# Kernel tuning notes

Measured on AMD Instinct MI355X. Metric: run time of the kernel, lower is better.

The kernel has to match this reference:

```python
import jax, jax.numpy as jnp
import numpy as np

B, S, D = 2, 2048, 1024
H, HD = 16, 64
DFF = 4 * D
EPS = 1e-5


def gelu(x):
    return 0.5 * x * (1.0 + jnp.tanh(jnp.sqrt(2.0 / jnp.pi) * (x + 0.044715 * x * x * x)))


def layer_norm(x, scale, bias):
    mu = jnp.mean(x, axis=-1, keepdims=True)
    var = jnp.mean(jnp.square(x - mu), axis=-1, keepdims=True)
    return (x - mu) * jax.lax.rsqrt(var + EPS) * scale + bias


def setup_inputs() -> dict:
    key = jax.random.key(0)
    ks = jax.random.split(key, 8)
    s = 0.02
    x = jax.random.normal(ks[0], (B, S, D), jnp.float32)
    mask = jnp.tril(jnp.ones((S, S), dtype=bool))[None, None]  # (1,1,S,S) causal
    return {
        "x": x,
        "mask": mask,
        "ln1_scale": jnp.ones((D,), jnp.float32),
        "ln1_bias": jnp.zeros((D,), jnp.float32),
        "ln2_scale": jnp.ones((D,), jnp.float32),
        "ln2_bias": jnp.zeros((D,), jnp.float32),
        "w_qkv": jax.random.normal(ks[1], (D, 3 * D), jnp.float32) * s,
        "b_qkv": jnp.zeros((3 * D,), jnp.float32),
        "w_attn_proj": jax.random.normal(ks[2], (D, D), jnp.float32) * s,
        "b_attn_proj": jnp.zeros((D,), jnp.float32),
        "w_fc": jax.random.normal(ks[3], (D, DFF), jnp.float32) * s,
        "b_fc": jnp.zeros((DFF,), jnp.float32),
        "w_mlp_proj": jax.random.normal(ks[4], (DFF, D), jnp.float32) * s,
        "b_mlp_proj": jnp.zeros((D,), jnp.float32),
    }


def reference(x, mask, ln1_scale, ln1_bias, ln2_scale, ln2_bias,
              w_qkv, b_qkv, w_attn_proj, b_attn_proj,
              w_fc, b_fc, w_mlp_proj, b_mlp_proj):
    bsz, seq, _ = x.shape
    # --- attention branch ---
    h = layer_norm(x, ln1_scale, ln1_bias)
    qkv = h @ w_qkv + b_qkv                       # (b, s, 3D)
    q, k, v = jnp.split(qkv, 3, axis=-1)
    q = q.reshape(bsz, seq, H, HD).transpose(0, 2, 1, 3)  # bhsd
    k = k.reshape(bsz, seq, H, HD).transpose(0, 2, 1, 3)
    v = v.reshape(bsz, seq, H, HD).transpose(0, 2, 1, 3)
    q = q * (1.0 / jnp.sqrt(HD))
    scores = jnp.einsum('bhqd,bhkd->bhqk', q, k)
    scores = jnp.where(mask, scores, -1e10)
    probs = jax.nn.softmax(scores, axis=-1)
    attn = jnp.einsum('bhqk,bhkd->bhqd', probs, v)
    attn = attn.transpose(0, 2, 1, 3).reshape(bsz, seq, D)
    attn = attn @ w_attn_proj + b_attn_proj
    x = x + attn
    # --- MLP branch ---
    h = layer_norm(x, ln2_scale, ln2_bias)
    h = gelu(h @ w_fc + b_fc)
    h = h @ w_mlp_proj + b_mlp_proj
    return x + h
```

## Files before the change

kernel.cpp:

```cpp
#include <hip/hip_runtime.h>
#include <stdint.h>


typedef __attribute__((ext_vector_type(8))) short bf16x8;
typedef __attribute__((ext_vector_type(8))) unsigned short u16x8;
typedef __attribute__((ext_vector_type(4))) float f32x4;

#define NEG_BIG -30000.0f
#define EXP2SC 0.18033688011112042f

__device__ __forceinline__ float b2f(unsigned short u) {
  union { unsigned int i; float f; } c; c.i = ((unsigned int)u) << 16; return c.f;
}
__device__ __forceinline__ unsigned short f2b(float f) {
  union { float f; unsigned int u; } c; c.f = f;
  unsigned int r = c.u + 0x7fffu + ((c.u >> 16) & 1u);
  return (unsigned short)(r >> 16);
}
__device__ __forceinline__ float ldx(const void* p, size_t i, int f32) {
  return f32 ? ((const float*)p)[i] : b2f(((const unsigned short*)p)[i]);
}
__device__ __forceinline__ void gld_lds16(const void* g, void* l) {
  __builtin_amdgcn_global_load_lds(
      (__attribute__((address_space(1))) void*)(void*)g,
      (__attribute__((address_space(3))) void*)l, 16, 0, 0);
}

__global__ void detect_k(const unsigned short* __restrict__ x, int* __restrict__ flag) {
  int lane = threadIdx.x;
  int cnt = 0;
#pragma unroll
  for (int j = 0; j < 4; ++j) {
    unsigned e = (x[lane * 4 + j] >> 7) & 0xFF;
    if (e >= 100 && e <= 145) cnt++;
  }
#pragma unroll
  for (int off = 32; off; off >>= 1) cnt += __shfl_down(cnt, off);
  if (lane == 0) *flag = (cnt < 220) ? 1 : 0;
}

__global__ __launch_bounds__(256) void transpose_k(
    const void* __restrict__ in, unsigned short* __restrict__ out,
    int K, int N, const int* __restrict__ flag) {
  int fm = *flag;
  __shared__ unsigned short tile[64][72];
  int n0 = blockIdx.x * 64, k0 = blockIdx.y * 64;
  int t = threadIdx.x;
  int r = t >> 3, c0 = (t & 7) * 8;
  if (fm) {
    const float* inf = (const float*)in;
#pragma unroll
    for (int p = 0; p < 2; ++p) {
      int k = r + p * 32;
      float4 v0 = *(const float4*)(inf + (size_t)(k0 + k) * N + n0 + c0);
      float4 v1 = *(const float4*)(inf + (size_t)(k0 + k) * N + n0 + c0 + 4);
      tile[k][c0 + 0] = f2b(v0.x); tile[k][c0 + 1] = f2b(v0.y);
      tile[k][c0 + 2] = f2b(v0.z); tile[k][c0 + 3] = f2b(v0.w);
      tile[k][c0 + 4] = f2b(v1.x); tile[k][c0 + 5] = f2b(v1.y);
      tile[k][c0 + 6] = f2b(v1.z); tile[k][c0 + 7] = f2b(v1.w);
    }
  } else {
    const unsigned short* inu = (const unsigned short*)in;
#pragma unroll
    for (int p = 0; p < 2; ++p) {
      int k = r + p * 32;
      u16x8 v = *(const u16x8*)(inu + (size_t)(k0 + k) * N + n0 + c0);
      *(u16x8*)&tile[k][c0] = v;
    }
  }
  __syncthreads();
#pragma unroll
  for (int p = 0; p < 2; ++p) {
    int n = r + p * 32;
    u16x8 v;
#pragma unroll
    for (int j = 0; j < 8; ++j) v[j] = tile[c0 + j][n];
    *(u16x8*)(out + (size_t)(n0 + n) * K + k0 + c0) = v;
  }
}

__global__ __launch_bounds__(256) void ln_k(
    const void* __restrict__ x, const void* __restrict__ sc,
    const void* __restrict__ bs, unsigned short* __restrict__ out,
    const int* __restrict__ flag, int xAdap) {
  int fm = *flag;
  int fx = xAdap ? fm : 0;
  int row = blockIdx.x, t = threadIdx.x;
  float f0, f1, f2, f3;
  if (fx) {
    float4 xv = ((const float4*)x)[(size_t)row * 256 + t];
    f0 = xv.x; f1 = xv.y; f2 = xv.z; f3 = xv.w;
  } else {
    ushort4 xv = ((const ushort4*)x)[(size_t)row * 256 + t];
    f0 = b2f(xv.x); f1 = b2f(xv.y); f2 = b2f(xv.z); f3 = b2f(xv.w);
  }
  float s = f0 + f1 + f2 + f3;
  float q = f0 * f0 + f1 * f1 + f2 * f2 + f3 * f3;
#pragma unroll
  for (int off = 32; off; off >>= 1) {
    s += __shfl_down(s, off);
    q += __shfl_down(q, off);
  }
  __shared__ float red[8];
  int w = t >> 6, lane = t & 63;
  if (lane == 0) { red[w] = s; red[w + 4] = q; }
  __syncthreads();
  float S = red[0] + red[1] + red[2] + red[3];
  float Q = red[4] + red[5] + red[6] + red[7];
  float mean = S * (1.f / 1024.f);
  float var = Q * (1.f / 1024.f) - mean * mean;
  float rstd = rsqrtf(var + 1e-5f);
  int c = t * 4;
  ushort4 o;
  o.x = f2b((f0 - mean) * rstd * ldx(sc, c, fm)     + ldx(bs, c, fm));
  o.y = f2b((f1 - mean) * rstd * ldx(sc, c + 1, fm) + ldx(bs, c + 1, fm));
  o.z = f2b((f2 - mean) * rstd * ldx(sc, c + 2, fm) + ldx(bs, c + 2, fm));
  o.w = f2b((f3 - mean) * rstd * ldx(sc, c + 3, fm) + ldx(bs, c + 3, fm));
  ((ushort4*)(out + (size_t)row * 1024))[t] = o;
}

template <int EPI>
__global__ __launch_bounds__(256) void gemm_bt(
    const unsigned short* __restrict__ A, const unsigned short* __restrict__ Bt,
    const void* __restrict__ bias, const void* __restrict__ res,
    void* __restrict__ C, int M, int N, int K,
    const int* __restrict__ flag, int resAdap, int outAdap) {
  int fm = *flag;
  int fr = resAdap ? fm : 0;
  int fo = outAdap ? fm : 0;
  __shared__ unsigned short As[2][128 * 32];
  __shared__ unsigned short Bs[2][128 * 32];
  int t = threadIdx.x;
  int bn = blockIdx.x * 128, bm = blockIdx.y * 128;
  int w = t >> 6, lane = t & 63, quad = lane >> 4, l16 = lane & 15;
  int wm = (w >> 1) * 64, wn = (w & 1) * 64;
  f32x4 acc[4][4] = {};

  int c1 = t, c2 = t + 256;
  int r1 = c1 >> 2, e1 = (c1 & 3) * 8;
  int r2 = c2 >> 2, e2 = (c2 & 3) * 8;
  const unsigned short* a1 = A + (size_t)(bm + r1) * K + e1;
  const unsigned short* a2 = A + (size_t)(bm + r2) * K + e2;
  const unsigned short* b1 = Bt + (size_t)(bn + r1) * K + e1;
  const unsigned short* b2 = Bt + (size_t)(bn + r2) * K + e2;

  for (int k0 = 0; k0 < K; k0 += 64) {
    gld_lds16(a1 + k0,      As[0] + c1 * 8);
    gld_lds16(a2 + k0,      As[0] + c2 * 8);
    gld_lds16(a1 + k0 + 32, As[1] + c1 * 8);
    gld_lds16(a2 + k0 + 32, As[1] + c2 * 8);
    gld_lds16(b1 + k0,      Bs[0] + c1 * 8);
    gld_lds16(b2 + k0,      Bs[0] + c2 * 8);
    gld_lds16(b1 + k0 + 32, Bs[1] + c1 * 8);
    gld_lds16(b2 + k0 + 32, Bs[1] + c2 * 8);
    __syncthreads();
#pragma unroll
    for (int h = 0; h < 2; ++h) {
      bf16x8 af[4], bfr[4];
#pragma unroll
      for (int i = 0; i < 4; ++i)
        af[i] = *(const bf16x8*)&As[h][(wm + i * 16 + l16) * 32 + quad * 8];
#pragma unroll
      for (int j = 0; j < 4; ++j)
        bfr[j] = *(const bf16x8*)&Bs[h][(wn + j * 16 + l16) * 32 + quad * 8];
#pragma unroll
      for (int i = 0; i < 4; ++i)
#pragma unroll
        for (int j = 0; j < 4; ++j)
          acc[i][j] = __builtin_amdgcn_mfma_f32_16x16x32_bf16(af[i], bfr[j], acc[i][j], 0, 0, 0);
    }
    __syncthreads();
  }

#pragma unroll
  for (int j = 0; j < 4; ++j) {
    int col = bn + wn + j * 16 + l16;
    float bb = ldx(bias, col, fm);
#pragma unroll
    for (int i = 0; i < 4; ++i) {
      int row0 = bm + wm + i * 16 + quad * 4;
#pragma unroll
      for (int r = 0; r < 4; ++r) {
        float v = acc[i][j][r] + bb;
        if (EPI == 1) {
          float u = 0.7978845608f * (v + 0.044715f * v * v * v);
          float e = __expf(2.f * u);
          float th = 1.f - 2.f / (e + 1.f);
          v = 0.5f * v * (1.f + th);
        } else if (EPI == 2) {
          v += ldx(res, (size_t)(row0 + r) * N + col, fr);
        }
        size_t idx = (size_t)(row0 + r) * N + col;
        if (fo) ((float*)C)[idx] = v;
        else    ((unsigned short*)C)[idx] = f2b(v);
      }
    }
  }
}

__global__ __launch_bounds__(256) void gemm_pk(
    const unsigned short* __restrict__ A, const unsigned short* __restrict__ Bt,
    float* __restrict__ P, int M, int N, int Kh, int Kfull) {
  __shared__ unsigned short As[2][128 * 32];
  __shared__ unsigned short Bs[2][128 * 32];
  int t = threadIdx.x;
  int bn = blockIdx.x * 128, bm = blockIdx.y * 128;
  int koff = blockIdx.z * Kh;
  float* Pz = P + (size_t)blockIdx.z * M * N;
  int w = t >> 6, lane = t & 63, quad = lane >> 4, l16 = lane & 15;
  int wm = (w >> 1) * 64, wn = (w & 1) * 64;
  f32x4 acc[4][4] = {};

  int c1 = t, c2 = t + 256;
  int r1 = c1 >> 2, e1 = (c1 & 3) * 8;
  int r2 = c2 >> 2, e2 = (c2 & 3) * 8;
  const unsigned short* a1 = A + (size_t)(bm + r1) * Kfull + koff + e1;
  const unsigned short* a2 = A + (size_t)(bm + r2) * Kfull + koff + e2;
  const unsigned short* b1 = Bt + (size_t)(bn + r1) * Kfull + koff + e1;
  const unsigned short* b2 = Bt + (size_t)(bn + r2) * Kfull + koff + e2;

  for (int k0 = 0; k0 < Kh; k0 += 64) {
    gld_lds16(a1 + k0,      As[0] + c1 * 8);
    gld_lds16(a2 + k0,      As[0] + c2 * 8);
    gld_lds16(a1 + k0 + 32, As[1] + c1 * 8);
    gld_lds16(a2 + k0 + 32, As[1] + c2 * 8);
    gld_lds16(b1 + k0,      Bs[0] + c1 * 8);
    gld_lds16(b2 + k0,      Bs[0] + c2 * 8);
    gld_lds16(b1 + k0 + 32, Bs[1] + c1 * 8);
    gld_lds16(b2 + k0 + 32, Bs[1] + c2 * 8);
    __syncthreads();
#pragma unroll
    for (int h = 0; h < 2; ++h) {
      bf16x8 af[4], bfr[4];
#pragma unroll
      for (int i = 0; i < 4; ++i)
        af[i] = *(const bf16x8*)&As[h][(wm + i * 16 + l16) * 32 + quad * 8];
#pragma unroll
      for (int j = 0; j < 4; ++j)
        bfr[j] = *(const bf16x8*)&Bs[h][(wn + j * 16 + l16) * 32 + quad * 8];
#pragma unroll
      for (int i = 0; i < 4; ++i)
#pragma unroll
        for (int j = 0; j < 4; ++j)
          acc[i][j] = __builtin_amdgcn_mfma_f32_16x16x32_bf16(af[i], bfr[j], acc[i][j], 0, 0, 0);
    }
    __syncthreads();
  }

#pragma unroll
  for (int j = 0; j < 4; ++j) {
    int col = bn + wn + j * 16 + l16;
#pragma unroll
    for (int i = 0; i < 4; ++i) {
      int row0 = bm + wm + i * 16 + quad * 4;
#pragma unroll
      for (int r = 0; r < 4; ++r)
        Pz[(size_t)(row0 + r) * N + col] = acc[i][j][r];
    }
  }
}

__global__ __launch_bounds__(256) void reduce2_k(
    const float* __restrict__ P0, const float* __restrict__ P1,
    const void* __restrict__ bias, const void* __restrict__ res,
    void* __restrict__ out, int N,
    const int* __restrict__ flag, int resAdap, int outAdap) {
  int fm = *flag;
  int fr = resAdap ? fm : 0;
  int fo = outAdap ? fm : 0;
  size_t idx = ((size_t)blockIdx.x * 256 + threadIdx.x) * 4;
  float4 p0 = *(const float4*)(P0 + idx);
  float4 p1 = *(const float4*)(P1 + idx);
  int col = (int)(idx & (size_t)(N - 1));
  float v0 = p0.x + p1.x + ldx(bias, col, fm)     + ldx(res, idx, fr);
  float v1 = p0.y + p1.y + ldx(bias, col + 1, fm) + ldx(res, idx + 1, fr);
  float v2 = p0.z + p1.z + ldx(bias, col + 2, fm) + ldx(res, idx + 2, fr);
  float v3 = p0.w + p1.w + ldx(bias, col + 3, fm) + ldx(res, idx + 3, fr);
  if (fo) {
    float4 o; o.x = v0; o.y = v1; o.z = v2; o.w = v3;
    *(float4*)((float*)out + idx) = o;
  } else {
    ushort4 o; o.x = f2b(v0); o.y = f2b(v1); o.z = f2b(v2); o.w = f2b(v3);
    *(ushort4*)((unsigned short*)out + idx) = o;
  }
}

__global__ __launch_bounds__(256) void attn_k(
    const unsigned short* __restrict__ qkv, unsigned short* __restrict__ out) {
  __shared__ unsigned short Ks[64 * 72];
  __shared__ unsigned int   Vt[64 * 35];
  __shared__ unsigned short Ps[4 * 16 * 72];
  int t = threadIdx.x, w = t >> 6, lane = t & 63, quad = lane >> 4, l16 = lane & 15;
  int qt = 31 - blockIdx.x, bh = blockIdx.y, b = bh >> 4, h = bh & 15;
  const unsigned short* base = qkv + (size_t)b * 2048 * 3072 + h * 64;
  unsigned short* Pw = Ps + w * 16 * 72;
  int srow = t >> 3, d0 = (t & 7) * 8;

  int q0 = qt * 64;
  int qrel = w * 16 + l16;
  const unsigned short* qp = base + (size_t)(q0 + qrel) * 3072;
  bf16x8 bq0 = *(const bf16x8*)(qp + quad * 8);
  bf16x8 bq1 = *(const bf16x8*)(qp + 32 + quad * 8);
  float m_i = NEG_BIG, l_i = 0.f;
  f32x4 O[4] = {};

#pragma unroll 1
  for (int kt = 0; kt <= qt; ++kt) {
    const unsigned short* kb = base + (size_t)(kt * 64) * 3072;
    {
      u16x8 k0v = *(const u16x8*)(kb + (size_t)srow * 3072 + 1024 + d0);
      u16x8 k1v = *(const u16x8*)(kb + (size_t)(srow + 32) * 3072 + 1024 + d0);
      *(u16x8*)&Ks[srow * 72 + d0] = k0v;
      *(u16x8*)&Ks[(srow + 32) * 72 + d0] = k1v;
      int sp = t >> 3;
      u16x8 va = *(const u16x8*)(kb + (size_t)(2 * sp) * 3072 + 2048 + d0);
      u16x8 vb = *(const u16x8*)(kb + (size_t)(2 * sp + 1) * 3072 + 2048 + d0);
#pragma unroll
      for (int j = 0; j < 8; ++j)
        Vt[(d0 + j) * 35 + sp] = (unsigned int)va[j] | ((unsigned int)vb[j] << 16);
    }
    __syncthreads();

    f32x4 ST[4];
#pragma unroll
    for (int i = 0; i < 4; ++i) {
      bf16x8 ak0 = *(const bf16x8*)&Ks[(i * 16 + l16) * 72 + quad * 8];
      bf16x8 ak1 = *(const bf16x8*)&Ks[(i * 16 + l16) * 72 + 32 + quad * 8];
      f32x4 z = {};
      z = __builtin_amdgcn_mfma_f32_16x16x32_bf16(ak0, bq0, z, 0, 0, 0);
      ST[i] = __builtin_amdgcn_mfma_f32_16x16x32_bf16(ak1, bq1, z, 0, 0, 0);
    }

    bool dm = (kt == qt);
    float p[4][4];
    float mx = NEG_BIG;
#pragma unroll
    for (int i = 0; i < 4; ++i)
#pragma unroll
      for (int r = 0; r < 4; ++r) {
        float v = ST[i][r] * EXP2SC;
        int srel = i * 16 + quad * 4 + r;
        if (dm && srel > qrel) v = NEG_BIG;
        p[i][r] = v;
        mx = fmaxf(mx, v);
      }
    mx = fmaxf(mx, __shfl_xor(mx, 16));
    mx = fmaxf(mx, __shfl_xor(mx, 32));
    float mn = fmaxf(m_i, mx);
    float alpha = exp2f(m_i - mn);
    m_i = mn;
    float sum = 0.f;
#pragma unroll
    for (int i = 0; i < 4; ++i)
#pragma unroll
      for (int r = 0; r < 4; ++r) {
        float e = exp2f(p[i][r] - mn);
        p[i][r] = e;
        sum += e;
      }
    sum += __shfl_xor(sum, 16);
    sum += __shfl_xor(sum, 32);
    l_i = alpha * l_i + sum;

#pragma unroll
    for (int i = 0; i < 4; ++i) {
      uint2 pr;
      pr.x = (unsigned int)f2b(p[i][0]) | ((unsigned int)f2b(p[i][1]) << 16);
      pr.y = (unsigned int)f2b(p[i][2]) | ((unsigned int)f2b(p[i][3]) << 16);
      *(uint2*)(Pw + l16 * 72 + i * 16 + quad * 4) = pr;
    }

    float ar[4];
#pragma unroll
    for (int r = 0; r < 4; ++r)
      ar[r] = __shfl(alpha, (lane & 48) | (quad * 4 + r));
#pragma unroll
    for (int jd = 0; jd < 4; ++jd)
#pragma unroll
      for (int r = 0; r < 4; ++r) O[jd][r] *= ar[r];

#pragma unroll
    for (int ks = 0; ks < 2; ++ks) {
      bf16x8 ap = *(const bf16x8*)(Pw + l16 * 72 + ks * 32 + quad * 8);
#pragma unroll
      for (int jd = 0; jd < 4; ++jd) {
        union { unsigned int u[4]; bf16x8 v; } bv;
        int vbase = (jd * 16 + l16) * 35 + ks * 16 + quad * 4;
#pragma unroll
        for (int cc = 0; cc < 4; ++cc) bv.u[cc] = Vt[vbase + cc];
        O[jd] = __builtin_amdgcn_mfma_f32_16x16x32_bf16(ap, bv.v, O[jd], 0, 0, 0);
      }
    }
    __syncthreads();
  }

  float li[4];
#pragma unroll
  for (int r = 0; r < 4; ++r)
    li[r] = 1.f / __shfl(l_i, (lane & 48) | (quad * 4 + r));
#pragma unroll
  for (int jd = 0; jd < 4; ++jd)
#pragma unroll
    for (int r = 0; r < 4; ++r) {
      size_t row = (size_t)b * 2048 + q0 + w * 16 + quad * 4 + r;
      out[row * 1024 + h * 64 + jd * 16 + l16] = f2b(O[jd][r] * li[r]);
    }
}

extern "C" void kernel_launch(void* const* d_in, const int* in_sizes, int n_in,
                              void* d_out, int out_size, void* d_ws, size_t ws_size,
                              hipStream_t stream) {
  (void)in_sizes; (void)n_in; (void)out_size;
  const void* x     = d_in[0];
  const void* ln1s  = d_in[2];
  const void* ln1b  = d_in[3];
  const void* ln2s  = d_in[4];
  const void* ln2b  = d_in[5];
  const void* w_qkv = d_in[6];
  const void* b_qkv = d_in[7];
  const void* w_ap  = d_in[8];
  const void* b_ap  = d_in[9];
  const void* w_fc  = d_in[10];
  const void* b_fc  = d_in[11];
  const void* w_mp  = d_in[12];
  const void* b_mp  = d_in[13];
  char* ws = (char*)d_ws;

  const int M = 4096, D = 1024, DFF = 4096, QKV3 = 3072;
  size_t off = 0;
  auto alloc = [&](size_t n) { char* p = ws + off; off += n; return p; };
  int* flag            = (int*)alloc(256);
  unsigned short* wT   = (unsigned short*)alloc((size_t)DFF * D * 2);
  unsigned short* hbuf = (unsigned short*)alloc((size_t)M * D * 2);
  unsigned short* x1   = (unsigned short*)alloc((size_t)M * D * 2);
  char* region = alloc((size_t)M * DFF * 2);
  unsigned short* qkvb = (unsigned short*)region;
  float* P0a = (float*)region;
  float* P1a = (float*)(region + (size_t)M * D * 4);
  unsigned short* fcb  = (unsigned short*)region;
  bool mlpSplit = ws_size >= off + (size_t)M * D * 8 + 1024;
  float* P0m = (float*)(ws + off);
  float* P1m = P0m + (size_t)M * D;

  dim3 blk(256);
  detect_k<<<dim3(1), dim3(64), 0, stream>>>((const unsigned short*)x, flag);
  transpose_k<<<dim3(QKV3 / 64, D / 64), blk, 0, stream>>>(w_qkv, wT, D, QKV3, flag);
  ln_k<<<dim3(M), blk, 0, stream>>>(x, ln1s, ln1b, hbuf, flag, 1);
  gemm_bt<0><<<dim3(QKV3 / 128, M / 128), blk, 0, stream>>>(hbuf, wT, b_qkv, nullptr, qkvb, M, QKV3, D, flag, 0, 0);
  attn_k<<<dim3(32, 32), blk, 0, stream>>>(qkvb, hbuf);
  transpose_k<<<dim3(D / 64, D / 64), blk, 0, stream>>>(w_ap, wT, D, D, flag);
  gemm_pk<<<dim3(D / 128, M / 128, 2), blk, 0, stream>>>(hbuf, wT, P0a, M, D, D / 2, D);
  reduce2_k<<<dim3(M * D / 1024), blk, 0, stream>>>(P0a, P1a, b_ap, x, x1, D, flag, 1, 0);
  transpose_k<<<dim3(DFF / 64, D / 64), blk, 0, stream>>>(w_fc, wT, D, DFF, flag);
  ln_k<<<dim3(M), blk, 0, stream>>>(x1, ln2s, ln2b, hbuf, flag, 0);
  gemm_bt<1><<<dim3(DFF / 128, M / 128), blk, 0, stream>>>(hbuf, wT, b_fc, nullptr, fcb, M, DFF, D, flag, 0, 0);
  transpose_k<<<dim3(D / 64, DFF / 64), blk, 0, stream>>>(w_mp, wT, DFF, D, flag);
  if (mlpSplit) {
    gemm_pk<<<dim3(D / 128, M / 128, 2), blk, 0, stream>>>(fcb, wT, P0m, M, D, DFF / 2, DFF);
    reduce2_k<<<dim3(M * D / 1024), blk, 0, stream>>>(P0m, P1m, b_mp, x1, d_out, D, flag, 0, 1);
  } else {
    gemm_bt<2><<<dim3(D / 128, M / 128), blk, 0, stream>>>(fcb, wT, b_mp, x1, d_out, M, D, DFF, flag, 0, 1);
  }
}
```

Measured before the change: 460.1 us.

## Pair causal query tiles per block and prefetch next K/V tile into registers

Each attention block now processes two query tiles (pi and 31-pi) so causal work is balanced across blocks, and the grid is halved to 16x32. The next K/V tile is loaded from global memory into registers while the current tile is being computed, which overlaps load latency with MFMA and softmax work. The bf16 packing of probabilities now uses the hardware-friendly __float22bfloat162_rn conversion. The cost is fewer blocks (512) and more live registers, which may lower occupancy.

```diff
diff --git a/kernel.cpp b/kernel.cpp
--- a/kernel.cpp
+++ b/kernel.cpp
@@ -1,4 +1,5 @@
 #include <hip/hip_runtime.h>
+#include <hip/hip_bf16.h>
 #include <stdint.h>
 
 
@@ -16,6 +17,12 @@
   union { float f; unsigned int u; } c; c.f = f;
   unsigned int r = c.u + 0x7fffu + ((c.u >> 16) & 1u);
   return (unsigned short)(r >> 16);
+}
+__device__ __forceinline__ unsigned int pk2bf(float a, float b) {
+  float2 f; f.x = a; f.y = b;
+  union { __hip_bfloat162 h; unsigned int u; } c;
+  c.h = __float22bfloat162_rn(f);
+  return c.u;
 }
 __device__ __forceinline__ float ldx(const void* p, size_t i, int f32) {
   return f32 ? ((const float*)p)[i] : b2f(((const unsigned short*)p)[i]);
@@ -291,120 +298,133 @@
   __shared__ unsigned int   Vt[64 * 35];
   __shared__ unsigned short Ps[4 * 16 * 72];
   int t = threadIdx.x, w = t >> 6, lane = t & 63, quad = lane >> 4, l16 = lane & 15;
-  int qt = 31 - blockIdx.x, bh = blockIdx.y, b = bh >> 4, h = bh & 15;
+  int pi = blockIdx.x, bh = blockIdx.y, b = bh >> 4, h = bh & 15;
   const unsigned short* base = qkv + (size_t)b * 2048 * 3072 + h * 64;
   unsigned short* Pw = Ps + w * 16 * 72;
   int srow = t >> 3, d0 = (t & 7) * 8;
 
-  int q0 = qt * 64;
-  int qrel = w * 16 + l16;
-  const unsigned short* qp = base + (size_t)(q0 + qrel) * 3072;
-  bf16x8 bq0 = *(const bf16x8*)(qp + quad * 8);
-  bf16x8 bq1 = *(const bf16x8*)(qp + 32 + quad * 8);
-  float m_i = NEG_BIG, l_i = 0.f;
-  f32x4 O[4] = {};
-
 #pragma unroll 1
-  for (int kt = 0; kt <= qt; ++kt) {
-    const unsigned short* kb = base + (size_t)(kt * 64) * 3072;
+  for (int half = 0; half < 2; ++half) {
+    int qt = half ? (31 - pi) : pi;
+    int q0 = qt * 64;
+    int qrel = w * 16 + l16;
+    const unsigned short* qp = base + (size_t)(q0 + qrel) * 3072;
+    bf16x8 bq0 = *(const bf16x8*)(qp + quad * 8);
+    bf16x8 bq1 = *(const bf16x8*)(qp + 32 + quad * 8);
+    float m_i = NEG_BIG, l_i = 0.f;
+    f32x4 O[4] = {};
+
+    u16x8 kA, kB, vA, vB;
     {
-      u16x8 k0v = *(const u16x8*)(kb + (size_t)srow * 3072 + 1024 + d0);
-      u16x8 k1v = *(const u16x8*)(kb + (size_t)(srow + 32) * 3072 + 1024 + d0);
-      *(u16x8*)&Ks[srow * 72 + d0] = k0v;
-      *(u16x8*)&Ks[(srow + 32) * 72 + d0] = k1v;
-      int sp = t >> 3;
-      u16x8 va = *(const u16x8*)(kb + (size_t)(2 * sp) * 3072 + 2048 + d0);
-      u16x8 vb = *(const u16x8*)(kb + (size_t)(2 * sp + 1) * 3072 + 2048 + d0);
+      const unsigned short* kb = base;
+      kA = *(const u16x8*)(kb + (size_t)srow * 3072 + 1024 + d0);
+      kB = *(const u16x8*)(kb + (size_t)(srow + 32) * 3072 + 1024 + d0);
+      vA = *(const u16x8*)(kb + (size_t)(2 * srow) * 3072 + 2048 + d0);
+      vB = *(const u16x8*)(kb + (size_t)(2 * srow + 1) * 3072 + 2048 + d0);
+    }
+
+#pragma unroll 1
+    for (int kt = 0; kt <= qt; ++kt) {
+      *(u16x8*)&Ks[srow * 72 + d0] = kA;
+      *(u16x8*)&Ks[(srow + 32) * 72 + d0] = kB;
 #pragma unroll
       for (int j = 0; j < 8; ++j)
-        Vt[(d0 + j) * 35 + sp] = (unsigned int)va[j] | ((unsigned int)vb[j] << 16);
-    }
-    __syncthreads();
-
-    f32x4 ST[4];
-#pragma unroll
-    for (int i = 0; i < 4; ++i) {
-      bf16x8 ak0 = *(const bf16x8*)&Ks[(i * 16 + l16) * 72 + quad * 8];
-      bf16x8 ak1 = *(const bf16x8*)&Ks[(i * 16 + l16) * 72 + 32 + quad * 8];
-      f32x4 z = {};
-      z = __builtin_amdgcn_mfma_f32_16x16x32_bf16(ak0, bq0, z, 0, 0, 0);
-      ST[i] = __builtin_amdgcn_mfma_f32_16x16x32_bf16(ak1, bq1, z, 0, 0, 0);
-    }
-
-    bool dm = (kt == qt);
-    float p[4][4];
-    float mx = NEG_BIG;
-#pragma unroll
-    for (int i = 0; i < 4; ++i)
+        Vt[(d0 + j) * 35 + srow] = (unsigned int)vA[j] | ((unsigned int)vB[j] << 16);
+      __syncthreads();
+
+      if (kt < qt) {
+        const unsigned short* kb = base + (size_t)((kt + 1) * 64) * 3072;
+        kA = *(const u16x8*)(kb + (size_t)srow * 3072 + 1024 + d0);
+        kB = *(const u16x8*)(kb + (size_t)(srow + 32) * 3072 + 1024 + d0);
+        vA = *(const u16x8*)(kb + (size_t)(2 * srow) * 3072 + 2048 + d0);
+        vB = *(const u16x8*)(kb + (size_t)(2 * srow + 1) * 3072 + 2048 + d0);
+      }
+
+      f32x4 ST[4];
+#pragma unroll
+      for (int i = 0; i < 4; ++i) {
+        bf16x8 ak0 = *(const bf16x8*)&Ks[(i * 16 + l16) * 72 + quad * 8];
+        bf16x8 ak1 = *(const bf16x8*)&Ks[(i * 16 + l16) * 72 + 32 + quad * 8];
+        f32x4 z = {};
+        z = __builtin_amdgcn_mfma_f32_16x16x32_bf16(ak0, bq0, z, 0, 0, 0);
+        ST[i] = __builtin_amdgcn_mfma_f32_16x16x32_bf16(ak1, bq1, z, 0, 0, 0);
+      }
+
+      bool dm = (kt == qt);
+      float p[4][4];
+      float mx = NEG_BIG;
+#pragma unroll
+      for (int i = 0; i < 4; ++i)
+#pragma unroll
+        for (int r = 0; r < 4; ++r) {
+          float v = ST[i][r] * EXP2SC;
+          int srel = i * 16 + quad * 4 + r;
+          if (dm && srel > qrel) v = NEG_BIG;
+          p[i][r] = v;
+          mx = fmaxf(mx, v);
+        }
+      mx = fmaxf(mx, __shfl_xor(mx, 16));
+      mx = fmaxf(mx, __shfl_xor(mx, 32));
+      float mn = fmaxf(m_i, mx);
+      float alpha = exp2f(m_i - mn);
+      m_i = mn;
+      float sum = 0.f;
+#pragma unroll
+      for (int i = 0; i < 4; ++i)
+#pragma unroll
+        for (int r = 0; r < 4; ++r) {
+          float e = exp2f(p[i][r] - mn);
+          p[i][r] = e;
+          sum += e;
+        }
+      sum += __shfl_xor(sum, 16);
+      sum += __shfl_xor(sum, 32);
+      l_i = alpha * l_i + sum;
+
+#pragma unroll
+      for (int i = 0; i < 4; ++i) {
+        uint2 pr;
+        pr.x = pk2bf(p[i][0], p[i][1]);
+        pr.y = pk2bf(p[i][2], p[i][3]);
+        *(uint2*)(Pw + l16 * 72 + i * 16 + quad * 4) = pr;
+      }
+
+      float ar[4];
+#pragma unroll
+      for (int r = 0; r < 4; ++r)
+        ar[r] = __shfl(alpha, (lane & 48) | (quad * 4 + r));
+#pragma unroll
+      for (int jd = 0; jd < 4; ++jd)
+#pragma unroll
+        for (int r = 0; r < 4; ++r) O[jd][r] *= ar[r];
+
+#pragma unroll
+      for (int ks = 0; ks < 2; ++ks) {
+        bf16x8 ap = *(const bf16x8*)(Pw + l16 * 72 + ks * 32 + quad * 8);
+#pragma unroll
+        for (int jd = 0; jd < 4; ++jd) {
+          union { unsigned int u[4]; bf16x8 v; } bv;
+          int vbase = (jd * 16 + l16) * 35 + ks * 16 + quad * 4;
+#pragma unroll
+          for (int cc = 0; cc < 4; ++cc) bv.u[cc] = Vt[vbase + cc];
+          O[jd] = __builtin_amdgcn_mfma_f32_16x16x32_bf16(ap, bv.v, O[jd], 0, 0, 0);
+        }
+      }
+      __syncthreads();
+    }
+
+    float li[4];
+#pragma unroll
+    for (int r = 0; r < 4; ++r)
+      li[r] = 1.f / __shfl(l_i, (lane & 48) | (quad * 4 + r));
+#pragma unroll
+    for (int jd = 0; jd < 4; ++jd)
 #pragma unroll
       for (int r = 0; r < 4; ++r) {
-        float v = ST[i][r] * EXP2SC;
-        int srel = i * 16 + quad * 4 + r;
-        if (dm && srel > qrel) v = NEG_BIG;
-        p[i][r] = v;
-        mx = fmaxf(mx, v);
-      }
-    mx = fmaxf(mx, __shfl_xor(mx, 16));
-    mx = fmaxf(mx, __shfl_xor(mx, 32));
-    float mn = fmaxf(m_i, mx);
-    float alpha = exp2f(m_i - mn);
-    m_i = mn;
-    float sum = 0.f;
-#pragma unroll
-    for (int i = 0; i < 4; ++i)
-#pragma unroll
-      for (int r = 0; r < 4; ++r) {
-        float e = exp2f(p[i][r] - mn);
-        p[i][r] = e;
-        sum += e;
-      }
-    sum += __shfl_xor(sum, 16);
-    sum += __shfl_xor(sum, 32);
-    l_i = alpha * l_i + sum;
-
-#pragma unroll
-    for (int i = 0; i < 4; ++i) {
-      uint2 pr;
-      pr.x = (unsigned int)f2b(p[i][0]) | ((unsigned int)f2b(p[i][1]) << 16);
-      pr.y = (unsigned int)f2b(p[i][2]) | ((unsigned int)f2b(p[i][3]) << 16);
-      *(uint2*)(Pw + l16 * 72 + i * 16 + quad * 4) = pr;
-    }
-
-    float ar[4];
-#pragma unroll
-    for (int r = 0; r < 4; ++r)
-      ar[r] = __shfl(alpha, (lane & 48) | (quad * 4 + r));
-#pragma unroll
-    for (int jd = 0; jd < 4; ++jd)
-#pragma unroll
-      for (int r = 0; r < 4; ++r) O[jd][r] *= ar[r];
-
-#pragma unroll
-    for (int ks = 0; ks < 2; ++ks) {
-      bf16x8 ap = *(const bf16x8*)(Pw + l16 * 72 + ks * 32 + quad * 8);
-#pragma unroll
-      for (int jd = 0; jd < 4; ++jd) {
-        union { unsigned int u[4]; bf16x8 v; } bv;
-        int vbase = (jd * 16 + l16) * 35 + ks * 16 + quad * 4;
-#pragma unroll
-        for (int cc = 0; cc < 4; ++cc) bv.u[cc] = Vt[vbase + cc];
-        O[jd] = __builtin_amdgcn_mfma_f32_16x16x32_bf16(ap, bv.v, O[jd], 0, 0, 0);
-      }
-    }
-    __syncthreads();
-  }
-
-  float li[4];
-#pragma unroll
-  for (int r = 0; r < 4; ++r)
-    li[r] = 1.f / __shfl(l_i, (lane & 48) | (quad * 4 + r));
-#pragma unroll
-  for (int jd = 0; jd < 4; ++jd)
-#pragma unroll
-    for (int r = 0; r < 4; ++r) {
-      size_t row = (size_t)b * 2048 + q0 + w * 16 + quad * 4 + r;
-      out[row * 1024 + h * 64 + jd * 16 + l16] = f2b(O[jd][r] * li[r]);
-    }
+        size_t row = (size_t)b * 2048 + q0 + w * 16 + quad * 4 + r;
+        out[row * 1024 + h * 64 + jd * 16 + l16] = f2b(O[jd][r] * li[r]);
+      }
+  }
 }
 
 extern "C" void kernel_launch(void* const* d_in, const int* in_sizes, int n_in,
@@ -447,7 +467,7 @@
   transpose_k<<<dim3(QKV3 / 64, D / 64), blk, 0, stream>>>(w_qkv, wT, D, QKV3, flag);
   ln_k<<<dim3(M), blk, 0, stream>>>(x, ln1s, ln1b, hbuf, flag, 1);
   gemm_bt<0><<<dim3(QKV3 / 128, M / 128), blk, 0, stream>>>(hbuf, wT, b_qkv, nullptr, qkvb, M, QKV3, D, flag, 0, 0);
-  attn_k<<<dim3(32, 32), blk, 0, stream>>>(qkvb, hbuf);
+  attn_k<<<dim3(16, 32), blk, 0, stream>>>(qkvb, hbuf);
   transpose_k<<<dim3(D / 64, D / 64), blk, 0, stream>>>(w_ap, wT, D, D, flag);
   gemm_pk<<<dim3(D / 128, M / 128, 2), blk, 0, stream>>>(hbuf, wT, P0a, M, D, D / 2, D);
   reduce2_k<<<dim3(M * D / 1024), blk, 0, stream>>>(P0a, P1a, b_ap, x, x1, D, flag, 1, 0);
```

Result: faster. 417.4 us (-9.3%).
